# Performance work log

Measured on AMD Instinct MI355X. Metric: run time of the kernel, lower is better.

Reference implementation:

```python
import jax, jax.numpy as jnp
import numpy as np

N = 100000
IN_CH = 128
OUT_CH = 128
H = 8
C = OUT_CH // H  # 16
K = 27  # kernel volume = 3**3
M = 1600000
BN_EPS = 1e-5


def _bn(x, gamma, beta):
    # training-mode BatchNorm1d over batch dim (biased variance)
    mu = x.mean(axis=0)
    var = x.var(axis=0)
    return (x - mu) * jax.lax.rsqrt(var + BN_EPS) * gamma + beta


def _l2norm(x):
    n = jnp.sqrt(jnp.sum(x * x, axis=-1, keepdims=True))
    return x / jnp.maximum(n, 1e-12)


def setup_inputs() -> dict:
    key = jax.random.key(0)
    ks = jax.random.split(key, 24)
    feats = jax.random.normal(ks[0], (N, IN_CH), jnp.float32)
    points = jax.random.normal(ks[1], (N, 3), jnp.float32)
    key_idx = jax.random.randint(ks[2], (M,), 0, N)
    kern_idx = jax.random.randint(ks[3], (M,), 0, K)
    q_idx = jax.random.randint(ks[4], (M,), 0, N)
    kq_map = jnp.stack([key_idx * K + kern_idx, q_idx]).astype(jnp.int32)
    s = 0.05
    params = dict(
        W1=jax.random.normal(ks[5], (3, 3), jnp.float32) * s,
        g1=jnp.ones((3,), jnp.float32), b1=jnp.zeros((3,), jnp.float32),
        W2=jax.random.normal(ks[6], (3, IN_CH), jnp.float32) * s,
        g2=jnp.ones((IN_CH,), jnp.float32), b2=jnp.zeros((IN_CH,), jnp.float32),
        W3=jax.random.normal(ks[7], (IN_CH, IN_CH), jnp.float32) * s,
        b3=jnp.zeros((IN_CH,), jnp.float32),
        Wq=jax.random.normal(ks[8], (IN_CH, OUT_CH), jnp.float32) * s,
        bq=jnp.zeros((OUT_CH,), jnp.float32),
        Wv=jax.random.normal(ks[9], (IN_CH, OUT_CH), jnp.float32) * s,
        bv=jnp.zeros((OUT_CH,), jnp.float32),
        pos_enc=jax.random.normal(ks[10], (K, H, C), jnp.float32),
        Wo=jax.random.normal(ks[11], (OUT_CH, OUT_CH), jnp.float32) * s,
        bo=jnp.zeros((OUT_CH,), jnp.float32),
    )
    return dict(feats=feats, points=points, kq_map=kq_map, **params)


def reference(feats, points, kq_map, W1, g1, b1, W2, g2, b2, W3, b3,
              Wq, bq, Wv, bv, pos_enc, Wo, bo):
    # intra-voxel positional MLP
    h = jax.nn.relu(_bn(points @ W1, g1, b1))
    h = jax.nn.relu(_bn(h @ W2, g2, b2))
    intra = h @ W3 + b3
    x = feats + intra  # [N, in_ch]
    q = (x @ Wq + bq).reshape(N, H, C)
    v = (x @ Wv + bv).reshape(N, H, C)
    nq = _l2norm(q)
    npe = _l2norm(pos_enc)  # [K, H, C]
    kern_idx = kq_map[0] % K
    key_idx = kq_map[0] // K
    q_idx = kq_map[1]
    # cosine-sim scores per map entry: [M, H]
    attn = jnp.einsum('mhc,mhc->mh', nq[q_idx], npe[kern_idx])
    # scatter weighted values to queries
    msg = attn[:, :, None] * v[key_idx]  # [M, H, C]
    out = jax.ops.segment_sum(msg, q_idx, num_segments=N)  # [N, H, C]
    out = out.reshape(N, OUT_CH) @ Wo + bo
    return out
```

## Files before the change

kernel.cpp:

```cpp
#include <hip/hip_runtime.h>
#include <hip/hip_bf16.h>
#include <stdint.h>


typedef unsigned short u16;
typedef __attribute__((ext_vector_type(8))) u16 u16x8;
typedef __attribute__((ext_vector_type(8))) short short8;
typedef __attribute__((ext_vector_type(4))) float f32x4;

#define CH 128
#define KVOL 27
#define CAP 64
#define LSTR 136
#define BN_EPS 1e-5f

__device__ __forceinline__ float bits2f(u16 u) {
  return __uint_as_float(((unsigned int)u) << 16);
}
__device__ __forceinline__ u16 f2bits(float x) {
  __hip_bfloat16 h = __float2bfloat16(x);
  return *reinterpret_cast<u16*>(&h);
}
__device__ __forceinline__ float ldf(const void* p, int i, bool bf) {
  return bf ? bits2f(((const u16*)p)[i]) : ((const float*)p)[i];
}
template <bool BF16>
__device__ __forceinline__ float ld(const void* p, int i) {
  if (BF16) return bits2f(((const u16*)p)[i]);
  return ((const float*)p)[i];
}

__global__ void detect_kernel(const void* g1, int* flag) {
  if (threadIdx.x == 0) flag[0] = (((const unsigned*)g1)[0] == 0x3F803F80u) ? 1 : 0;
}

__global__ void prep_all(const void* W3, const void* Wq, const void* Wv, const void* Wo,
                         const void* b3, const void* bq, const void* bv, const void* bo,
                         const void* pos_enc,
                         u16* W3T, u16* WqT, u16* WvT, u16* WoT,
                         float* b3f, float* bqf, float* bvf, float* bof,
                         float* npe, const int* flag) {
  bool bf = (*flag != 0);
  int bid = blockIdx.x, t = threadIdx.x;
  if (bid < 256) {
    int idx = bid * 256 + t;
    int sel = idx >> 14;
    int r = idx & (CH * CH - 1);
    int k = r >> 7, n = r & 127;
    const void* src = (sel == 0) ? W3 : (sel == 1) ? Wq : (sel == 2) ? Wv : Wo;
    u16*       dst = (sel == 0) ? W3T : (sel == 1) ? WqT : (sel == 2) ? WvT : WoT;
    dst[n * CH + k] = f2bits(ldf(src, k * CH + n, bf));
  } else if (bid == 256) {
    for (int idx = t; idx < 4 * CH; idx += 256) {
      int which = idx >> 7, j = idx & 127;
      const void* src = (which == 0) ? b3 : (which == 1) ? bq : (which == 2) ? bv : bo;
      float* dst = (which == 0) ? b3f : (which == 1) ? bqf : (which == 2) ? bvf : bof;
      dst[j] = ldf(src, j, bf);
    }
  } else {
    int k = bid - 257;
    if (t < CH) {
      float val = ldf(pos_enc, k * CH + t, bf);
      float ss = val * val;
      ss += __shfl_xor(ss, 1); ss += __shfl_xor(ss, 2);
      ss += __shfl_xor(ss, 4); ss += __shfl_xor(ss, 8);
      npe[k * CH + t] = val / fmaxf(sqrtf(ss), 1e-12f);
    }
  }
}

template <bool BF16>
__device__ void stats1_body(const void* points, const void* W1, float* stats1, int N,
                            float red[4][6]) {
  float w[9];
#pragma unroll
  for (int i = 0; i < 9; i++) w[i] = ld<BF16>(W1, i);
  float s[3] = {0.f, 0.f, 0.f}, ss[3] = {0.f, 0.f, 0.f};
  for (int p = blockIdx.x * blockDim.x + threadIdx.x; p < N; p += gridDim.x * blockDim.x) {
    float a0 = ld<BF16>(points, p * 3 + 0);
    float a1 = ld<BF16>(points, p * 3 + 1);
    float a2 = ld<BF16>(points, p * 3 + 2);
#pragma unroll
    for (int i = 0; i < 3; i++) {
      float v = a0 * w[i] + a1 * w[3 + i] + a2 * w[6 + i];
      s[i] += v; ss[i] += v * v;
    }
  }
#pragma unroll
  for (int i = 0; i < 3; i++) {
    for (int off = 32; off; off >>= 1) {
      s[i] += __shfl_down(s[i], off);
      ss[i] += __shfl_down(ss[i], off);
    }
  }
  int wave = threadIdx.x >> 6;
  if ((threadIdx.x & 63) == 0) {
#pragma unroll
    for (int i = 0; i < 3; i++) { red[wave][i] = s[i]; red[wave][3 + i] = ss[i]; }
  }
  __syncthreads();
  if (threadIdx.x == 0) {
#pragma unroll
    for (int i = 0; i < 6; i++) {
      float acc = red[0][i] + red[1][i] + red[2][i] + red[3][i];
      atomicAdd(&stats1[i], acc);
    }
  }
}
__global__ void stats1_kernel(const void* points, const void* W1, float* stats1, int N,
                              const int* flag) {
  __shared__ float red[4][6];
  if (*flag) stats1_body<true>(points, W1, stats1, N, red);
  else       stats1_body<false>(points, W1, stats1, N, red);
}

template <bool BF16>
__device__ void stats2_body(const void* points, const void* W1, const void* g1,
                            const void* b1, const void* W2, const float* stats1,
                            float* stats2, int N, float sh_s[2][CH], float sh_q[2][CH]) {
  int j = threadIdx.x & 127, psub = threadIdx.x >> 7;
  float w1[9];
#pragma unroll
  for (int i = 0; i < 9; i++) w1[i] = ld<BF16>(W1, i);
  float invN = 1.0f / (float)N;
  float s1[3], o1[3];
#pragma unroll
  for (int i = 0; i < 3; i++) {
    float mu = stats1[i] * invN;
    float var = stats1[3 + i] * invN - mu * mu;
    float sc = ld<BF16>(g1, i) * rsqrtf(var + BN_EPS);
    s1[i] = sc; o1[i] = ld<BF16>(b1, i) - mu * sc;
  }
  float w2c[3];
#pragma unroll
  for (int a = 0; a < 3; a++) w2c[a] = ld<BF16>(W2, a * CH + j);
  float sum = 0.f, ssum = 0.f;
  for (int p = blockIdx.x * 2 + psub; p < N; p += gridDim.x * 2) {
    float a0 = ld<BF16>(points, p * 3 + 0);
    float a1 = ld<BF16>(points, p * 3 + 1);
    float a2 = ld<BF16>(points, p * 3 + 2);
    float h2 = 0.f;
#pragma unroll
    for (int i = 0; i < 3; i++) {
      float p1 = a0 * w1[i] + a1 * w1[3 + i] + a2 * w1[6 + i];
      float h1 = fmaxf(p1 * s1[i] + o1[i], 0.f);
      h2 += h1 * w2c[i];
    }
    sum += h2; ssum += h2 * h2;
  }
  sh_s[psub][j] = sum; sh_q[psub][j] = ssum;
  __syncthreads();
  if (psub == 0) {
    atomicAdd(&stats2[j], sum + sh_s[1][j]);
    atomicAdd(&stats2[CH + j], ssum + sh_q[1][j]);
  }
}
__global__ void stats2_kernel(const void* points, const void* W1, const void* g1,
                              const void* b1, const void* W2, const float* stats1,
                              float* stats2, int N, const int* flag) {
  __shared__ float sh_s[2][CH], sh_q[2][CH];
  if (*flag) stats2_body<true>(points, W1, g1, b1, W2, stats1, stats2, N, sh_s, sh_q);
  else       stats2_body<false>(points, W1, g1, b1, W2, stats1, stats2, N, sh_s, sh_q);
}

__device__ __forceinline__ void gemm_core128(const u16* sA, const u16* sB,
                                             f32x4 acc[2][8], int wave, int lane) {
  int q = lane >> 4, r = lane & 15;
  int rowA0 = (wave * 32 + r) * LSTR;
  int rowA1 = (wave * 32 + 16 + r) * LSTR;
#pragma unroll
  for (int ks = 0; ks < 4; ks++) {
    int kk = ks * 32 + q * 8;
    short8 a0 = *(const short8*)&sA[rowA0 + kk];
    short8 a1 = *(const short8*)&sA[rowA1 + kk];
#pragma unroll
    for (int c = 0; c < 8; c++) {
      short8 b = *(const short8*)&sB[(c * 16 + r) * LSTR + kk];
      acc[0][c] = __builtin_amdgcn_mfma_f32_16x16x32_bf16(a0, b, acc[0][c], 0, 0, 0);
      acc[1][c] = __builtin_amdgcn_mfma_f32_16x16x32_bf16(a1, b, acc[1][c], 0, 0, 0);
    }
  }
}
__device__ __forceinline__ void stage_w(const u16* Wg, u16* sB, int tid) {
  for (int chk = tid; chk < 2048; chk += 256) {
    int n = chk >> 4, c = chk & 15;
    *(u16x8*)&sB[n * LSTR + c * 8] = *(const u16x8*)&Wg[n * CH + c * 8];
  }
}
__device__ __forceinline__ void zero_acc(f32x4 acc[2][8]) {
#pragma unroll
  for (int wm = 0; wm < 2; wm++)
#pragma unroll
    for (int c = 0; c < 8; c++) acc[wm][c] = (f32x4){0.f, 0.f, 0.f, 0.f};
}
__device__ __forceinline__ void cvals_to_lds(const f32x4 acc[2][8], const float* bias,
                                             u16* dst, int wave, int q, int r) {
#pragma unroll
  for (int wm = 0; wm < 2; wm++) {
#pragma unroll
    for (int c = 0; c < 8; c++) {
      int col = c * 16 + r;
      float bj = bias[col];
#pragma unroll
      for (int i = 0; i < 4; i++) {
        int lrow = wave * 32 + wm * 16 + q * 4 + i;
        dst[lrow * LSTR + col] = f2bits(acc[wm][c][i] + bj);
      }
    }
  }
}

__global__ __launch_bounds__(256)
void fused_qv_kernel(const void* points, const void* feats,
                     const void* W1, const void* g1, const void* b1,
                     const void* W2, const void* g2, const void* b2,
                     const u16* W3T, const u16* WqT, const u16* WvT,
                     const float* b3f, const float* bqf, const float* bvf,
                     const float* st1, const float* st2,
                     u16* nq16, u16* v16, int N, const int* flag) {
  __shared__ __align__(16) u16 sA[128 * LSTR];
  __shared__ __align__(16) u16 sB[128 * LSTR];
  __shared__ float s_pts[128 * 3];
  bool bf = (*flag != 0);
  int tid = threadIdx.x;
  int m0 = blockIdx.x * 128;
  int lane = tid & 63, wave = tid >> 6;
  int q = lane >> 4, r = lane & 15;

  for (int idx = tid; idx < 128 * 3; idx += 256) {
    int g = m0 * 3 + idx;
    s_pts[idx] = (g < N * 3) ? ldf(points, g, bf) : 0.f;
  }
  stage_w(W3T, sB, tid);
  __syncthreads();

  {
    int j = tid & 127, psub = tid >> 7;
    float w1[9];
#pragma unroll
    for (int i = 0; i < 9; i++) w1[i] = ldf(W1, i, bf);
    float invN = 1.0f / (float)N;
    float s1[3], o1[3];
#pragma unroll
    for (int i = 0; i < 3; i++) {
      float mu = st1[i] * invN;
      float var = st1[3 + i] * invN - mu * mu;
      float sc = ldf(g1, i, bf) * rsqrtf(var + BN_EPS);
      s1[i] = sc; o1[i] = ldf(b1, i, bf) - mu * sc;
    }
    float w2c[3];
#pragma unroll
    for (int a = 0; a < 3; a++) w2c[a] = ldf(W2, a * CH + j, bf);
    float mu2 = st2[j] * invN;
    float var2 = st2[CH + j] * invN - mu2 * mu2;
    float s2 = ldf(g2, j, bf) * rsqrtf(var2 + BN_EPS);
    float o2 = ldf(b2, j, bf) - mu2 * s2;
#pragma unroll 4
    for (int e = 0; e < 64; e++) {
      int m = psub + e * 2;
      float a0 = s_pts[m * 3 + 0];
      float a1 = s_pts[m * 3 + 1];
      float a2 = s_pts[m * 3 + 2];
      float h2 = 0.f;
#pragma unroll
      for (int i = 0; i < 3; i++) {
        float p1 = a0 * w1[i] + a1 * w1[3 + i] + a2 * w1[6 + i];
        float h1 = fmaxf(p1 * s1[i] + o1[i], 0.f);
        h2 += h1 * w2c[i];
      }
      sA[m * LSTR + j] = f2bits(fmaxf(h2 * s2 + o2, 0.f));
    }
  }
  __syncthreads();

  f32x4 acc[2][8];
  zero_acc(acc);
  gemm_core128(sA, sB, acc, wave, lane);
  cvals_to_lds(acc, b3f, sA, wave, q, r);
  __syncthreads();
  for (int chk = tid; chk < 2048; chk += 256) {
    int m = chk >> 4, c = chk & 15;
    int grow = m0 + m;
    if (grow < N) {
      u16x8 xv = *(const u16x8*)&sA[m * LSTR + c * 8];
      float fv[8];
      if (bf) {
        u16x8 fw = *(const u16x8*)((const u16*)feats + (size_t)grow * CH + c * 8);
#pragma unroll
        for (int k = 0; k < 8; k++) fv[k] = bits2f(fw[k]);
      } else {
        const float* fp = (const float*)feats + (size_t)grow * CH + c * 8;
        f32x4 f0 = *(const f32x4*)fp;
        f32x4 f1 = *(const f32x4*)(fp + 4);
#pragma unroll
        for (int k = 0; k < 4; k++) { fv[k] = f0[k]; fv[4 + k] = f1[k]; }
      }
      u16x8 outv;
#pragma unroll
      for (int k = 0; k < 8; k++) outv[k] = f2bits(bits2f(xv[k]) + fv[k]);
      *(u16x8*)&sA[m * LSTR + c * 8] = outv;
    }
  }
  stage_w(WqT, sB, tid);
  __syncthreads();

  zero_acc(acc);
  gemm_core128(sA, sB, acc, wave, lane);
  float nvals[2][8][4];
#pragma unroll
  for (int wm = 0; wm < 2; wm++) {
#pragma unroll
    for (int c = 0; c < 8; c++) {
      float bj = bqf[c * 16 + r];
#pragma unroll
      for (int i = 0; i < 4; i++) {
        float v = acc[wm][c][i] + bj;
        float ss = v * v;
        ss += __shfl_xor(ss, 1); ss += __shfl_xor(ss, 2);
        ss += __shfl_xor(ss, 4); ss += __shfl_xor(ss, 8);
        nvals[wm][c][i] = v / fmaxf(sqrtf(ss), 1e-12f);
      }
    }
  }
  __syncthreads();
#pragma unroll
  for (int wm = 0; wm < 2; wm++)
#pragma unroll
    for (int c = 0; c < 8; c++)
#pragma unroll
      for (int i = 0; i < 4; i++) {
        int lrow = wave * 32 + wm * 16 + q * 4 + i;
        sB[lrow * LSTR + c * 16 + r] = f2bits(nvals[wm][c][i]);
      }
  __syncthreads();
  for (int chk = tid; chk < 2048; chk += 256) {
    int m = chk >> 4, c = chk & 15;
    int grow = m0 + m;
    if (grow < N)
      *(u16x8*)&nq16[(size_t)grow * CH + c * 8] = *(const u16x8*)&sB[m * LSTR + c * 8];
  }
  __syncthreads();
  stage_w(WvT, sB, tid);
  __syncthreads();

  zero_acc(acc);
  gemm_core128(sA, sB, acc, wave, lane);
  __syncthreads();
  cvals_to_lds(acc, bvf, sB, wave, q, r);
  __syncthreads();
  for (int chk = tid; chk < 2048; chk += 256) {
    int m = chk >> 4, c = chk & 15;
    int grow = m0 + m;
    if (grow < N)
      *(u16x8*)&v16[(size_t)grow * CH + c * 8] = *(const u16x8*)&sB[m * LSTR + c * 8];
  }
}

__global__ __launch_bounds__(256)
void gemm_out_kernel(const u16* __restrict__ A, const u16* __restrict__ WoT,
                     const float* __restrict__ bof, void* __restrict__ out,
                     int N, const int* flag) {
  __shared__ __align__(16) u16 sA[128 * LSTR];
  __shared__ __align__(16) u16 sB[128 * LSTR];
  bool bf = (*flag != 0);
  int tid = threadIdx.x;
  int m0 = blockIdx.x * 128;
  int lane = tid & 63, wave = tid >> 6;
  int q = lane >> 4, r = lane & 15;
  stage_w(WoT, sB, tid);
  for (int chk = tid; chk < 2048; chk += 256) {
    int m = chk >> 4, c = chk & 15;
    int gm = m0 + m;
    u16x8 val = {0, 0, 0, 0, 0, 0, 0, 0};
    if (gm < N) val = *(const u16x8*)&A[(size_t)gm * CH + c * 8];
    *(u16x8*)&sA[m * LSTR + c * 8] = val;
  }
  __syncthreads();
  f32x4 acc[2][8];
  zero_acc(acc);
  gemm_core128(sA, sB, acc, wave, lane);
  __syncthreads();
  cvals_to_lds(acc, bof, sB, wave, q, r);
  __syncthreads();
  for (int chk = tid; chk < 2048; chk += 256) {
    int m = chk >> 4, c = chk & 15;
    int grow = m0 + m;
    if (grow < N) {
      u16x8 v = *(const u16x8*)&sB[m * LSTR + c * 8];
      if (bf) {
        *(u16x8*)((u16*)out + (size_t)grow * CH + c * 8) = v;
      } else {
        float* op = (float*)out + (size_t)grow * CH + c * 8;
        f32x4 f0, f1;
#pragma unroll
        for (int k = 0; k < 4; k++) { f0[k] = bits2f(v[k]); f1[k] = bits2f(v[4 + k]); }
        *(f32x4*)op = f0;
        *(f32x4*)(op + 4) = f1;
      }
    }
  }
}

__global__ void fill_kernel(const int* __restrict__ kq0, const int* __restrict__ kq1,
                            int* __restrict__ counts, int* __restrict__ bucket,
                            int M, int N) {
  int g = blockIdx.x & 7;
  int qlo = (int)(((long long)N * g) >> 3);
  int qhi = (int)(((long long)N * (g + 1)) >> 3);
  int nb = gridDim.x >> 3;
  int ib = blockIdx.x >> 3;
  int stride = nb * blockDim.x;
  for (int m = ib * blockDim.x + threadIdx.x; m < M; m += stride) {
    int q = kq1[m];
    int c0 = kq0[m];
    if (q >= qlo && q < qhi) {
      int pos = atomicAdd(&counts[q], 1);
      if (pos < CAP) bucket[q * CAP + pos] = c0;
    }
  }
}

__global__ void attn_kernel(const float* __restrict__ npe, const u16* __restrict__ nq16,
                            const u16* __restrict__ v16, const int* __restrict__ counts,
                            const int* __restrict__ bucket, u16* __restrict__ segsum) {
  __shared__ float s_nq[CH];
  __shared__ float s_sc[CAP][8];
  __shared__ int s_key[CAP], s_e[CAP];
  __shared__ float s_par[2][CH];
  int n = blockIdx.x, t = threadIdx.x;
  int cnt = counts[n];
  cnt = (cnt > CAP) ? CAP : cnt;
  if (t < cnt) {
    int c0 = bucket[n * CAP + t];
    int key = c0 / KVOL;
    s_key[t] = key;
    s_e[t] = c0 - key * KVOL;
  }
  s_nq[t] = bits2f(nq16[n * CH + t]);
  __syncthreads();
  int tot = cnt << 3;
  for (int base = 0; base < tot; base += 128) {
    int idx = base + t;
    if (idx < tot) {
      int i = idx >> 3, h = idx & 7;
      const float* pe = &npe[s_e[i] * CH + h * 16];
      const float* nn = &s_nq[h * 16];
      float s = 0.f;
#pragma unroll
      for (int c = 0; c < 16; c += 4) {
        f32x4 p = *(const f32x4*)(pe + c);
        f32x4 nv = *(const f32x4*)(nn + c);
#pragma unroll
        for (int k = 0; k < 4; k++) s = fmaf(nv[k], p[k], s);
      }
      s_sc[i][h] = s;
    }
  }
  __syncthreads();
  int w = t >> 6, l = t & 63;
  int h = l >> 3;
  float a0 = 0.f, a1 = 0.f;
  int i = w;
  for (; i + 2 < cnt; i += 4) {
    unsigned g0 = *(const unsigned*)&v16[(size_t)s_key[i] * CH + 2 * l];
    unsigned g1 = *(const unsigned*)&v16[(size_t)s_key[i + 2] * CH + 2 * l];
    float sc0 = s_sc[i][h], sc1 = s_sc[i + 2][h];
    a0 = fmaf(sc0, bits2f((u16)(g0 & 0xffff)), a0);
    a1 = fmaf(sc0, bits2f((u16)(g0 >> 16)), a1);
    a0 = fmaf(sc1, bits2f((u16)(g1 & 0xffff)), a0);
    a1 = fmaf(sc1, bits2f((u16)(g1 >> 16)), a1);
  }
  if (i < cnt) {
    unsigned g0 = *(const unsigned*)&v16[(size_t)s_key[i] * CH + 2 * l];
    float sc0 = s_sc[i][h];
    a0 = fmaf(sc0, bits2f((u16)(g0 & 0xffff)), a0);
    a1 = fmaf(sc0, bits2f((u16)(g0 >> 16)), a1);
  }
  s_par[w][2 * l] = a0;
  s_par[w][2 * l + 1] = a1;
  __syncthreads();
  if (t < 64) {
    float r0 = s_par[0][2 * t] + s_par[1][2 * t];
    float r1 = s_par[0][2 * t + 1] + s_par[1][2 * t + 1];
    unsigned o = (unsigned)f2bits(r0) | ((unsigned)f2bits(r1) << 16);
    *(unsigned*)&segsum[(size_t)n * CH + 2 * t] = o;
  }
}

extern "C" void kernel_launch(void* const* d_in, const int* in_sizes, int n_in,
                              void* d_out, int out_size, void* d_ws, size_t ws_size,
                              hipStream_t stream) {
  const void* feats   = d_in[0];
  const void* points  = d_in[1];
  const int*  kq      = (const int*)d_in[2];
  const void* W1      = d_in[3];
  const void* g1      = d_in[4];
  const void* b1      = d_in[5];
  const void* W2      = d_in[6];
  const void* g2      = d_in[7];
  const void* b2      = d_in[8];
  const void* W3      = d_in[9];
  const void* b3      = d_in[10];
  const void* Wq      = d_in[11];
  const void* bq      = d_in[12];
  const void* Wv      = d_in[13];
  const void* bv      = d_in[14];
  const void* pos_enc = d_in[15];
  const void* Wo      = d_in[16];
  const void* bo      = d_in[17];

  const int N = in_sizes[0] / CH;
  const int M = in_sizes[2] / 2;
  const int* kq0 = kq;
  const int* kq1 = kq + M;

  char* ws = (char*)d_ws;
  size_t off = 0;
  auto alloc = [&](size_t bytes) -> void* {
    void* p = ws + off;
    off = (off + bytes + 255) & ~(size_t)255;
    return p;
  };
  int*   flag   = (int*)alloc(sizeof(int));
  float* npe    = (float*)alloc(KVOL * CH * sizeof(float));
  u16*   W3T    = (u16*)alloc(CH * CH * sizeof(u16));
  u16*   WqT    = (u16*)alloc(CH * CH * sizeof(u16));
  u16*   WvT    = (u16*)alloc(CH * CH * sizeof(u16));
  u16*   WoT    = (u16*)alloc(CH * CH * sizeof(u16));
  float* b3f    = (float*)alloc(CH * sizeof(float));
  float* bqf    = (float*)alloc(CH * sizeof(float));
  float* bvf    = (float*)alloc(CH * sizeof(float));
  float* bof    = (float*)alloc(CH * sizeof(float));
  float* stats  = (float*)alloc((8 + 2 * CH) * sizeof(float));
  float* st1    = stats;
  float* st2    = stats + 8;
  u16*   nqbuf  = (u16*)alloc((size_t)N * CH * sizeof(u16));
  u16*   vbuf   = (u16*)alloc((size_t)N * CH * sizeof(u16));
  u16*   segbuf = (u16*)alloc((size_t)N * CH * sizeof(u16));
  int*   counts = (int*)alloc((size_t)N * sizeof(int));
  int*   bucket = (int*)alloc((size_t)N * CAP * sizeof(int));

  hipMemsetAsync(stats, 0, (8 + 2 * CH) * sizeof(float), stream);
  hipMemsetAsync(counts, 0, (size_t)N * sizeof(int), stream);

  detect_kernel<<<1, 64, 0, stream>>>(g1, flag);
  prep_all<<<257 + KVOL, 256, 0, stream>>>(W3, Wq, Wv, Wo, b3, bq, bv, bo, pos_enc,
                                           W3T, WqT, WvT, WoT, b3f, bqf, bvf, bof,
                                           npe, flag);
  stats1_kernel<<<128, 256, 0, stream>>>(points, W1, st1, N, flag);
  stats2_kernel<<<2048, 256, 0, stream>>>(points, W1, g1, b1, W2, st1, st2, N, flag);
  fill_kernel<<<1024, 256, 0, stream>>>(kq0, kq1, counts, bucket, M, N);

  int gblocks = (N + 127) / 128;
  fused_qv_kernel<<<gblocks, 256, 0, stream>>>(points, feats, W1, g1, b1, W2, g2, b2,
                                               W3T, WqT, WvT, b3f, bqf, bvf, st1, st2,
                                               nqbuf, vbuf, N, flag);
  attn_kernel<<<N, CH, 0, stream>>>(npe, nqbuf, vbuf, counts, bucket, segbuf);
  gemm_out_kernel<<<gblocks, 256, 0, stream>>>(segbuf, WoT, bof, d_out, N, flag);
}
```

Baseline: 499.3 us.

## Split bucket fill into per-slice counters and replace stats2 atomics with partials

The fill kernel used to have each of 8 block groups scan all M entries and keep only its query range. Now each group handles one eighth of M and writes to private counters and sub-buckets per slice. A pack kernel merges the per-slice counts into one u64 per query, and the attention kernel builds a compacted edge list from them. The stats2 float atomics become per-block partials reduced by a single-block kernel, and the gather loop is unrolled to four keys per wave. This removes the 8x redundant read of the map but costs a larger bucket array, extra memsets and two extra launches, and each slice may now drop entries past 16.

```diff
diff --git a/kernel.cpp b/kernel.cpp
--- a/kernel.cpp
+++ b/kernel.cpp
@@ -4,13 +4,15 @@
 
 
 typedef unsigned short u16;
+typedef unsigned long long u64;
 typedef __attribute__((ext_vector_type(8))) u16 u16x8;
 typedef __attribute__((ext_vector_type(8))) short short8;
 typedef __attribute__((ext_vector_type(4))) float f32x4;
 
 #define CH 128
 #define KVOL 27
-#define CAP 64
+#define SCAP 16
+#define MAXE 128
 #define LSTR 136
 #define BN_EPS 1e-5f
 
@@ -115,9 +117,9 @@
 }
 
 template <bool BF16>
-__device__ void stats2_body(const void* points, const void* W1, const void* g1,
-                            const void* b1, const void* W2, const float* stats1,
-                            float* stats2, int N, float sh_s[2][CH], float sh_q[2][CH]) {
+__device__ void stats2a_body(const void* points, const void* W1, const void* g1,
+                             const void* b1, const void* W2, const float* stats1,
+                             float* partials, int N, float sh_s[2][CH], float sh_q[2][CH]) {
   int j = threadIdx.x & 127, psub = threadIdx.x >> 7;
   float w1[9];
 #pragma unroll
@@ -151,16 +153,30 @@
   sh_s[psub][j] = sum; sh_q[psub][j] = ssum;
   __syncthreads();
   if (psub == 0) {
-    atomicAdd(&stats2[j], sum + sh_s[1][j]);
-    atomicAdd(&stats2[CH + j], ssum + sh_q[1][j]);
-  }
-}
-__global__ void stats2_kernel(const void* points, const void* W1, const void* g1,
-                              const void* b1, const void* W2, const float* stats1,
-                              float* stats2, int N, const int* flag) {
+    partials[blockIdx.x * 256 + j] = sum + sh_s[1][j];
+    partials[blockIdx.x * 256 + 128 + j] = ssum + sh_q[1][j];
+  }
+}
+__global__ void stats2a_kernel(const void* points, const void* W1, const void* g1,
+                               const void* b1, const void* W2, const float* stats1,
+                               float* partials, int N, const int* flag) {
   __shared__ float sh_s[2][CH], sh_q[2][CH];
-  if (*flag) stats2_body<true>(points, W1, g1, b1, W2, stats1, stats2, N, sh_s, sh_q);
-  else       stats2_body<false>(points, W1, g1, b1, W2, stats1, stats2, N, sh_s, sh_q);
+  if (*flag) stats2a_body<true>(points, W1, g1, b1, W2, stats1, partials, N, sh_s, sh_q);
+  else       stats2a_body<false>(points, W1, g1, b1, W2, stats1, partials, N, sh_s, sh_q);
+}
+__global__ void stats2b_kernel(const float* __restrict__ partials, float* __restrict__ st2,
+                               int B) {
+  int t = threadIdx.x;
+  float a0 = 0.f, a1 = 0.f, a2 = 0.f, a3 = 0.f;
+  int b = 0;
+  for (; b + 4 <= B; b += 4) {
+    a0 += partials[(b + 0) * 256 + t];
+    a1 += partials[(b + 1) * 256 + t];
+    a2 += partials[(b + 2) * 256 + t];
+    a3 += partials[(b + 3) * 256 + t];
+  }
+  for (; b < B; b++) a0 += partials[b * 256 + t];
+  st2[t] = (a0 + a1) + (a2 + a3);
 }
 
 __device__ __forceinline__ void gemm_core128(const u16* sA, const u16* sB,
@@ -402,39 +418,62 @@
 }
 
 __global__ void fill_kernel(const int* __restrict__ kq0, const int* __restrict__ kq1,
-                            int* __restrict__ counts, int* __restrict__ bucket,
+                            int* __restrict__ counts8, int* __restrict__ bucket,
                             int M, int N) {
-  int g = blockIdx.x & 7;
-  int qlo = (int)(((long long)N * g) >> 3);
-  int qhi = (int)(((long long)N * (g + 1)) >> 3);
+  int j = blockIdx.x & 7;
+  int start = (int)(((long long)M * j) >> 3);
+  int end   = (int)(((long long)M * (j + 1)) >> 3);
   int nb = gridDim.x >> 3;
   int ib = blockIdx.x >> 3;
   int stride = nb * blockDim.x;
-  for (int m = ib * blockDim.x + threadIdx.x; m < M; m += stride) {
+  int* cnt = counts8 + (size_t)j * N;
+  for (int m = start + ib * blockDim.x + threadIdx.x; m < end; m += stride) {
     int q = kq1[m];
     int c0 = kq0[m];
-    if (q >= qlo && q < qhi) {
-      int pos = atomicAdd(&counts[q], 1);
-      if (pos < CAP) bucket[q * CAP + pos] = c0;
-    }
-  }
+    int pos = atomicAdd(&cnt[q], 1);
+    if (pos < SCAP) bucket[(size_t)q * 128 + j * SCAP + pos] = c0;
+  }
+}
+
+__global__ void counts_pack_kernel(const int* __restrict__ counts8,
+                                   u64* __restrict__ countsT, int N) {
+  int q = blockIdx.x * 256 + threadIdx.x;
+  if (q >= N) return;
+  u64 v = 0;
+#pragma unroll
+  for (int j = 0; j < 8; j++) {
+    int c = counts8[(size_t)j * N + q];
+    c = (c > SCAP) ? SCAP : c;
+    v |= (u64)c << (8 * j);
+  }
+  countsT[q] = v;
 }
 
 __global__ void attn_kernel(const float* __restrict__ npe, const u16* __restrict__ nq16,
-                            const u16* __restrict__ v16, const int* __restrict__ counts,
+                            const u16* __restrict__ v16, const u64* __restrict__ countsT,
                             const int* __restrict__ bucket, u16* __restrict__ segsum) {
   __shared__ float s_nq[CH];
-  __shared__ float s_sc[CAP][8];
-  __shared__ int s_key[CAP], s_e[CAP];
+  __shared__ float s_sc[MAXE][8];
+  __shared__ int s_key[MAXE], s_e[MAXE];
   __shared__ float s_par[2][CH];
   int n = blockIdx.x, t = threadIdx.x;
-  int cnt = counts[n];
-  cnt = (cnt > CAP) ? CAP : cnt;
-  if (t < cnt) {
-    int c0 = bucket[n * CAP + t];
-    int key = c0 / KVOL;
-    s_key[t] = key;
-    s_e[t] = c0 - key * KVOL;
+  u64 cv = countsT[n];
+  int c[8], off[8], cnt = 0;
+#pragma unroll
+  for (int j = 0; j < 8; j++) {
+    c[j] = (int)((cv >> (8 * j)) & 0xff);
+    off[j] = cnt;
+    cnt += c[j];
+  }
+  {
+    int j = t >> 4, idx = t & 15;
+    if (idx < c[j]) {
+      int c0 = bucket[(size_t)n * 128 + j * SCAP + idx];
+      int key = c0 / KVOL;
+      int pos = off[j] + idx;
+      s_key[pos] = key;
+      s_e[pos] = c0 - key * KVOL;
+    }
   }
   s_nq[t] = bits2f(nq16[n * CH + t]);
   __syncthreads();
@@ -447,9 +486,9 @@
       const float* nn = &s_nq[h * 16];
       float s = 0.f;
 #pragma unroll
-      for (int c = 0; c < 16; c += 4) {
-        f32x4 p = *(const f32x4*)(pe + c);
-        f32x4 nv = *(const f32x4*)(nn + c);
+      for (int cc = 0; cc < 16; cc += 4) {
+        f32x4 p = *(const f32x4*)(pe + cc);
+        f32x4 nv = *(const f32x4*)(nn + cc);
 #pragma unroll
         for (int k = 0; k < 4; k++) s = fmaf(nv[k], p[k], s);
       }
@@ -461,16 +500,23 @@
   int h = l >> 3;
   float a0 = 0.f, a1 = 0.f;
   int i = w;
-  for (; i + 2 < cnt; i += 4) {
+  for (; i + 6 < cnt; i += 8) {
     unsigned g0 = *(const unsigned*)&v16[(size_t)s_key[i] * CH + 2 * l];
     unsigned g1 = *(const unsigned*)&v16[(size_t)s_key[i + 2] * CH + 2 * l];
+    unsigned g2 = *(const unsigned*)&v16[(size_t)s_key[i + 4] * CH + 2 * l];
+    unsigned g3 = *(const unsigned*)&v16[(size_t)s_key[i + 6] * CH + 2 * l];
     float sc0 = s_sc[i][h], sc1 = s_sc[i + 2][h];
+    float sc2 = s_sc[i + 4][h], sc3 = s_sc[i + 6][h];
     a0 = fmaf(sc0, bits2f((u16)(g0 & 0xffff)), a0);
     a1 = fmaf(sc0, bits2f((u16)(g0 >> 16)), a1);
     a0 = fmaf(sc1, bits2f((u16)(g1 & 0xffff)), a0);
     a1 = fmaf(sc1, bits2f((u16)(g1 >> 16)), a1);
-  }
-  if (i < cnt) {
+    a0 = fmaf(sc2, bits2f((u16)(g2 & 0xffff)), a0);
+    a1 = fmaf(sc2, bits2f((u16)(g2 >> 16)), a1);
+    a0 = fmaf(sc3, bits2f((u16)(g3 & 0xffff)), a0);
+    a1 = fmaf(sc3, bits2f((u16)(g3 >> 16)), a1);
+  }
+  for (; i < cnt; i += 2) {
     unsigned g0 = *(const unsigned*)&v16[(size_t)s_key[i] * CH + 2 * l];
     float sc0 = s_sc[i][h];
     a0 = fmaf(sc0, bits2f((u16)(g0 & 0xffff)), a0);
@@ -521,40 +567,44 @@
     off = (off + bytes + 255) & ~(size_t)255;
     return p;
   };
-  int*   flag   = (int*)alloc(sizeof(int));
-  float* npe    = (float*)alloc(KVOL * CH * sizeof(float));
-  u16*   W3T    = (u16*)alloc(CH * CH * sizeof(u16));
-  u16*   WqT    = (u16*)alloc(CH * CH * sizeof(u16));
-  u16*   WvT    = (u16*)alloc(CH * CH * sizeof(u16));
-  u16*   WoT    = (u16*)alloc(CH * CH * sizeof(u16));
-  float* b3f    = (float*)alloc(CH * sizeof(float));
-  float* bqf    = (float*)alloc(CH * sizeof(float));
-  float* bvf    = (float*)alloc(CH * sizeof(float));
-  float* bof    = (float*)alloc(CH * sizeof(float));
-  float* stats  = (float*)alloc((8 + 2 * CH) * sizeof(float));
-  float* st1    = stats;
-  float* st2    = stats + 8;
-  u16*   nqbuf  = (u16*)alloc((size_t)N * CH * sizeof(u16));
-  u16*   vbuf   = (u16*)alloc((size_t)N * CH * sizeof(u16));
-  u16*   segbuf = (u16*)alloc((size_t)N * CH * sizeof(u16));
-  int*   counts = (int*)alloc((size_t)N * sizeof(int));
-  int*   bucket = (int*)alloc((size_t)N * CAP * sizeof(int));
-
-  hipMemsetAsync(stats, 0, (8 + 2 * CH) * sizeof(float), stream);
-  hipMemsetAsync(counts, 0, (size_t)N * sizeof(int), stream);
+  const int SB = 2048;
+  int*   flag    = (int*)alloc(sizeof(int));
+  float* npe     = (float*)alloc(KVOL * CH * sizeof(float));
+  u16*   W3T     = (u16*)alloc(CH * CH * sizeof(u16));
+  u16*   WqT     = (u16*)alloc(CH * CH * sizeof(u16));
+  u16*   WvT     = (u16*)alloc(CH * CH * sizeof(u16));
+  u16*   WoT     = (u16*)alloc(CH * CH * sizeof(u16));
+  float* b3f     = (float*)alloc(CH * sizeof(float));
+  float* bqf     = (float*)alloc(CH * sizeof(float));
+  float* bvf     = (float*)alloc(CH * sizeof(float));
+  float* bof     = (float*)alloc(CH * sizeof(float));
+  float* st1     = (float*)alloc(8 * sizeof(float));
+  float* st2     = (float*)alloc(2 * CH * sizeof(float));
+  float* part2   = (float*)alloc((size_t)SB * 256 * sizeof(float));
+  u16*   nqbuf   = (u16*)alloc((size_t)N * CH * sizeof(u16));
+  u16*   vbuf    = (u16*)alloc((size_t)N * CH * sizeof(u16));
+  u16*   segbuf  = (u16*)alloc((size_t)N * CH * sizeof(u16));
+  int*   counts8 = (int*)alloc((size_t)8 * N * sizeof(int));
+  u64*   countsT = (u64*)alloc((size_t)N * sizeof(u64));
+  int*   bucket  = (int*)alloc((size_t)N * 128 * sizeof(int));
+
+  hipMemsetAsync(st1, 0, 8 * sizeof(float), stream);
+  hipMemsetAsync(counts8, 0, (size_t)8 * N * sizeof(int), stream);
 
   detect_kernel<<<1, 64, 0, stream>>>(g1, flag);
   prep_all<<<257 + KVOL, 256, 0, stream>>>(W3, Wq, Wv, Wo, b3, bq, bv, bo, pos_enc,
                                            W3T, WqT, WvT, WoT, b3f, bqf, bvf, bof,
                                            npe, flag);
   stats1_kernel<<<128, 256, 0, stream>>>(points, W1, st1, N, flag);
-  stats2_kernel<<<2048, 256, 0, stream>>>(points, W1, g1, b1, W2, st1, st2, N, flag);
-  fill_kernel<<<1024, 256, 0, stream>>>(kq0, kq1, counts, bucket, M, N);
+  stats2a_kernel<<<SB, 256, 0, stream>>>(points, W1, g1, b1, W2, st1, part2, N, flag);
+  stats2b_kernel<<<1, 256, 0, stream>>>(part2, st2, SB);
+  fill_kernel<<<1024, 256, 0, stream>>>(kq0, kq1, counts8, bucket, M, N);
+  counts_pack_kernel<<<(N + 255) / 256, 256, 0, stream>>>(counts8, countsT, N);
 
   int gblocks = (N + 127) / 128;
   fused_qv_kernel<<<gblocks, 256, 0, stream>>>(points, feats, W1, g1, b1, W2, g2, b2,
                                                W3T, WqT, WvT, b3f, bqf, bvf, st1, st2,
                                                nqbuf, vbuf, N, flag);
-  attn_kernel<<<N, CH, 0, stream>>>(npe, nqbuf, vbuf, counts, bucket, segbuf);
+  attn_kernel<<<N, CH, 0, stream>>>(npe, nqbuf, vbuf, countsT, bucket, segbuf);
   gemm_out_kernel<<<gblocks, 256, 0, stream>>>(segbuf, WoT, bof, d_out, N, flag);
 }
```

Result: slower. 587.0 us (+17.5%).
